# Kernel optimization log

Hardware: AMD Instinct MI355X
Metric: run time of the kernel (lower is better)

The kernel has to match this reference:

```python
import jax, jax.numpy as jnp
import numpy as np

B, L, E = 4, 2048, 1024
H, D = 16, 64  # heads, head_dim; H*D == E


def setup_inputs() -> dict:
    key = jax.random.key(0)
    ks = jax.random.split(key, 6)
    s = 0.02
    return {
        "x": jax.random.normal(ks[0], (B, L, E), dtype=jnp.float32),
        "Wq": jax.random.normal(ks[1], (E, H * D), dtype=jnp.float32) * s,
        "Wk": jax.random.normal(ks[2], (E, H * D), dtype=jnp.float32) * s,
        "Wv": jax.random.normal(ks[3], (E, H * D), dtype=jnp.float32) * s,
        "Wo": jax.random.normal(ks[4], (H * D, E), dtype=jnp.float32) * s,
        "bo": jax.random.normal(ks[5], (E,), dtype=jnp.float32) * s,
    }


def reference(x, Wq, Wk, Wv, Wo, bo):
    b, l, e = x.shape
    q = (x @ Wq).reshape(b, l, H, D)
    k = (x @ Wk).reshape(b, l, H, D)
    v = (x @ Wv).reshape(b, l, H, D)
    # NOTE: original scales by sqrt(embed_size), not sqrt(head_dim)
    energy = jnp.einsum('nqhd,nkhd->nhqk', q, k)
    attn = jax.nn.softmax(energy / jnp.sqrt(jnp.float32(e)), axis=3)
    out = jnp.einsum('nhql,nlhd->nqhd', attn, v).reshape(b, l, H * D)
    return out @ Wo + bo
```

## Files before the change

kernel.cpp:

```cpp
#include <hip/hip_runtime.h>

#define B_ 4
#define L_ 2048
#define E_ 1024
#define H_ 16
#define D_ 64
#define CSCALE 0.045084960222629414f

typedef short s16x8 __attribute__((ext_vector_type(8)));
typedef short s16x4 __attribute__((ext_vector_type(4)));
typedef float f32x4 __attribute__((ext_vector_type(4)));

__device__ __forceinline__ unsigned short f2bf(float f) {
  union { float f; unsigned int u; } v;
  v.f = f;
  unsigned int u = v.u;
  u += 0x7fffu + ((u >> 16) & 1u);
  return (unsigned short)(u >> 16);
}

__device__ __forceinline__ void async16(const void* g, void* l) {
  __builtin_amdgcn_global_load_lds(
      (__attribute__((address_space(1))) void*)(g),
      (__attribute__((address_space(3))) void*)(l), 16, 0, 0);
}

__global__ void k_prep(const float* __restrict__ x,
                       const float* __restrict__ Wq, const float* __restrict__ Wk,
                       const float* __restrict__ Wv, const float* __restrict__ Wo,
                       unsigned short* __restrict__ xb,
                       unsigned short* __restrict__ Wt, unsigned short* __restrict__ WoT) {
  __shared__ float t[32][33];
  int bid = blockIdx.x, tid = threadIdx.x;
  if (bid < 8192) {
    int i = bid * 256 + tid;
    float4 v = ((const float4*)x)[i];
    ushort4 o;
    o.x = f2bf(v.x); o.y = f2bf(v.y); o.z = f2bf(v.z); o.w = f2bf(v.w);
    ((ushort4*)xb)[i] = o;
    return;
  }
  int tt = bid - 8192;
  int wsel = tt >> 10, tile = tt & 1023;
  const float* in = (wsel == 0) ? Wq : (wsel == 1) ? Wk : (wsel == 2) ? Wv : Wo;
  unsigned short* out = (wsel == 0) ? Wt : (wsel == 1) ? Wt + (1u << 20)
                        : (wsel == 2) ? Wt + (2u << 20) : WoT;
  int bx = tile & 31, by = tile >> 5;
  int tx = tid & 31, ty = tid >> 5;
  int xcol = bx * 32 + tx;
  int y0 = by * 32;
#pragma unroll
  for (int i = 0; i < 4; ++i)
    t[ty + i * 8][tx] = in[(size_t)(y0 + ty + i * 8) * 1024 + xcol];
  __syncthreads();
  int xo = by * 32 + tx;
  int yo0 = bx * 32;
#pragma unroll
  for (int i = 0; i < 4; ++i)
    out[(size_t)(yo0 + ty + i * 8) * 1024 + xo] = f2bf(t[tx][ty + i * 8]);
}

__global__ __launch_bounds__(256) void k_gemm_qkvt(
    const unsigned short* __restrict__ xb, const unsigned short* __restrict__ Wt,
    unsigned short* __restrict__ Qb, unsigned short* __restrict__ Kb,
    unsigned short* __restrict__ Vt) {
  __shared__ __align__(16) unsigned short As[128 * 32];
  __shared__ __align__(16) unsigned short Bs[128 * 32];
  const int bid = blockIdx.x;
  const int tid = threadIdx.x;
  const int w = tid >> 6, lane = tid & 63;
  const int quad = lane >> 4, mrow = lane & 15;
  const bool isQK = bid < 1024;
  int m0, n0;
  const unsigned short *PA, *PB;
  if (isQK) {
    m0 = (bid & 63) * 128;
    n0 = (bid >> 6) * 128;
    PA = xb + (size_t)m0 * 1024;
    PB = Wt + (size_t)n0 * 1024;
  } else {
    int g = bid - 1024;
    m0 = (g & 7) * 128;
    n0 = (g >> 3) * 128;
    PA = Wt + (2u << 20) + (size_t)m0 * 1024;
    PB = xb + (size_t)n0 * 1024;
  }
  const int wr = (w >> 1) * 64, wc = (w & 1) * 64;
  const f32x4 fz = {0.f, 0.f, 0.f, 0.f};
  f32x4 acc[4][4];
#pragma unroll
  for (int a = 0; a < 4; ++a)
#pragma unroll
    for (int b = 0; b < 4; ++b) acc[a][b] = fz;

  for (int kt = 0; kt < 32; ++kt) {
    __syncthreads();
#pragma unroll
    for (int r = 0; r < 2; ++r) {
      int c = r * 256 + tid;
      int row = c >> 2, cc = c & 3;
      async16(PA + (size_t)row * 1024 + kt * 32 + cc * 8, &As[c * 8]);
    }
#pragma unroll
    for (int r = 0; r < 2; ++r) {
      int c = r * 256 + tid;
      int row = c >> 2, cc = c & 3;
      async16(PB + (size_t)row * 1024 + kt * 32 + cc * 8, &Bs[c * 8]);
    }
    __syncthreads();
    s16x8 a[4], b[4];
#pragma unroll
    for (int mt = 0; mt < 4; ++mt)
      a[mt] = *(const s16x8*)&As[(wr + mt * 16 + mrow) * 32 + quad * 8];
#pragma unroll
    for (int nt = 0; nt < 4; ++nt)
      b[nt] = *(const s16x8*)&Bs[(wc + nt * 16 + mrow) * 32 + quad * 8];
#pragma unroll
    for (int mt = 0; mt < 4; ++mt)
#pragma unroll
      for (int nt = 0; nt < 4; ++nt)
        acc[mt][nt] = __builtin_amdgcn_mfma_f32_16x16x32_bf16(a[mt], b[nt], acc[mt][nt], 0, 0, 0);
  }
  if (isQK) {
#pragma unroll
    for (int mt = 0; mt < 4; ++mt)
#pragma unroll
      for (int nt = 0; nt < 4; ++nt)
#pragma unroll
        for (int i = 0; i < 4; ++i) {
          int row = m0 + wr + mt * 16 + quad * 4 + i;
          int col = n0 + wc + nt * 16 + mrow;
          int bb = row >> 11, l = row & 2047;
          if (col < 1024) {
            int h = col >> 6, d = col & 63;
            Qb[(((size_t)(bb * 16 + h)) * 2048 + l) * 64 + d] = f2bf(acc[mt][nt][i]);
          } else {
            int c2 = col - 1024, h = c2 >> 6, d = c2 & 63;
            Kb[(((size_t)(bb * 16 + h)) * 2048 + l) * 64 + d] = f2bf(acc[mt][nt][i] * CSCALE);
          }
        }
  } else {
#pragma unroll
    for (int mt = 0; mt < 4; ++mt)
#pragma unroll
      for (int nt = 0; nt < 4; ++nt)
#pragma unroll
        for (int i = 0; i < 4; ++i) {
          int f = m0 + wr + mt * 16 + quad * 4 + i;
          int tk = n0 + wc + nt * 16 + mrow;
          int bb = tk >> 11, l = tk & 2047;
          Vt[((size_t)(bb * 1024 + f)) * 2048 + l] = f2bf(acc[mt][nt][i]);
        }
  }
}

__global__ __launch_bounds__(512, 4) void k_attn(
    const unsigned short* __restrict__ Qb, const unsigned short* __restrict__ Kb,
    const unsigned short* __restrict__ Vt, unsigned short* __restrict__ AO) {
  __shared__ __align__(16) unsigned short KVs[2][8192];
  const int tid = threadIdx.x, w = tid >> 6, lane = tid & 63;
  const int quad = lane >> 4, mrow = lane & 15;
  const int bh = blockIdx.y;
  const int q0 = blockIdx.x * 256;
  const unsigned short* Qh = Qb + (size_t)bh * 2048 * 64;
  const unsigned short* Kh = Kb + (size_t)bh * 2048 * 64;
  const unsigned short* Vh = Vt + (size_t)bh * 64 * 2048;
  unsigned short* KVf = &KVs[0][0];

#pragma unroll
  for (int r = 0; r < 4; ++r) {
    int c = r * 512 + tid;
    int row = c >> 3, cl = c & 7;
    int gc = cl ^ (row & 7);
    async16(Qh + (size_t)(q0 + row) * 64 + gc * 8, &KVf[c * 8]);
  }
  __syncthreads();
  s16x8 qb[2][2];
#pragma unroll
  for (int nt = 0; nt < 2; ++nt)
#pragma unroll
    for (int ks = 0; ks < 2; ++ks) {
      int row = w * 32 + nt * 16 + mrow;
      qb[nt][ks] = *(const s16x8*)&KVf[row * 64 + (((ks * 4 + quad) ^ (row & 7)) << 3)];
    }
  __syncthreads();

  {
    int c = tid;
    int row = c >> 3, cl = c & 7;
    int gc = cl ^ (row & 7);
    async16(Kh + (size_t)row * 64 + gc * 8, &KVs[0][c * 8]);
    async16(Vh + (size_t)row * 2048 + gc * 8, &KVs[0][4096 + c * 8]);
  }

  const f32x4 fz = {0.f, 0.f, 0.f, 0.f};
  f32x4 o[2][4];
  float lr[2];
#pragma unroll
  for (int nt = 0; nt < 2; ++nt) {
    lr[nt] = 0.f;
#pragma unroll
    for (int dt = 0; dt < 4; ++dt) o[nt][dt] = fz;
  }

  for (int j = 0; j < 32; ++j) {
    __syncthreads();
    const unsigned short* Kt = &KVs[j & 1][0];
    const unsigned short* Vs = &KVs[j & 1][4096];

    s16x8 ak[4][2];
#pragma unroll
    for (int mt = 0; mt < 4; ++mt)
#pragma unroll
      for (int ks = 0; ks < 2; ++ks) {
        int row = mt * 16 + mrow;
        ak[mt][ks] = *(const s16x8*)&Kt[row * 64 + (((ks * 4 + quad) ^ (row & 7)) << 3)];
      }
    s16x4 vb[4][4];
#pragma unroll
    for (int dt = 0; dt < 4; ++dt)
#pragma unroll
      for (int lt = 0; lt < 4; ++lt) {
        int row = dt * 16 + mrow;
        int lbase = lt * 16 + quad * 4;
        int cg = lbase >> 3, off = lbase & 7;
        vb[dt][lt] = *(const s16x4*)&Vs[row * 64 + ((cg ^ (row & 7)) << 3) + off];
      }

    if (j + 1 < 32) {
      unsigned short* nb = &KVs[(j + 1) & 1][0];
      int c = tid;
      int row = c >> 3, cl = c & 7;
      int gc = cl ^ (row & 7);
      async16(Kh + (size_t)((j + 1) * 64 + row) * 64 + gc * 8, &nb[c * 8]);
      async16(Vh + (size_t)row * 2048 + (j + 1) * 64 + gc * 8, &nb[4096 + c * 8]);
    }

    f32x4 s[4][2];
#pragma unroll
    for (int mt = 0; mt < 4; ++mt)
#pragma unroll
      for (int nt = 0; nt < 2; ++nt) s[mt][nt] = fz;
    __builtin_amdgcn_s_setprio(1);
#pragma unroll
    for (int ks = 0; ks < 2; ++ks)
#pragma unroll
      for (int mt = 0; mt < 4; ++mt)
#pragma unroll
        for (int nt = 0; nt < 2; ++nt)
          s[mt][nt] = __builtin_amdgcn_mfma_f32_16x16x32_bf16(ak[mt][ks], qb[nt][ks], s[mt][nt], 0, 0, 0);
    __builtin_amdgcn_s_setprio(0);

    s16x4 pa[4][2];
#pragma unroll
    for (int mt = 0; mt < 4; ++mt)
#pragma unroll
      for (int nt = 0; nt < 2; ++nt) {
        float p0 = __builtin_amdgcn_exp2f(s[mt][nt][0]);
        float p1 = __builtin_amdgcn_exp2f(s[mt][nt][1]);
        float p2 = __builtin_amdgcn_exp2f(s[mt][nt][2]);
        float p3 = __builtin_amdgcn_exp2f(s[mt][nt][3]);
        lr[nt] += (p0 + p1) + (p2 + p3);
        unsigned int r01, r23;
        asm("v_cvt_pk_bf16_f32 %0, %1, %2" : "=v"(r01) : "v"(p0), "v"(p1));
        asm("v_cvt_pk_bf16_f32 %0, %1, %2" : "=v"(r23) : "v"(p2), "v"(p3));
        union { unsigned int u[2]; s16x4 v4; } uu;
        uu.u[0] = r01; uu.u[1] = r23;
        pa[mt][nt] = uu.v4;
      }

    __builtin_amdgcn_s_setprio(1);
#pragma unroll
    for (int nt = 0; nt < 2; ++nt)
#pragma unroll
      for (int dt = 0; dt < 4; ++dt)
#pragma unroll
        for (int lt = 0; lt < 4; ++lt)
          o[nt][dt] = __builtin_amdgcn_mfma_f32_16x16x16bf16_1k(pa[lt][nt], vb[dt][lt], o[nt][dt], 0, 0, 0);
    __builtin_amdgcn_s_setprio(0);
  }

#pragma unroll
  for (int nt = 0; nt < 2; ++nt) {
    float v = lr[nt];
    v += __shfl_xor(v, 16);
    v += __shfl_xor(v, 32);
    lr[nt] = v;
  }

  int b_ = bh >> 4, h = bh & 15;
#pragma unroll
  for (int nt = 0; nt < 2; ++nt)
#pragma unroll
    for (int i = 0; i < 4; ++i) {
      float inv = 1.f / __shfl(lr[nt], quad * 4 + i, 64);
      int qrow = q0 + w * 32 + nt * 16 + quad * 4 + i;
#pragma unroll
      for (int dt = 0; dt < 4; ++dt) {
        int d = dt * 16 + mrow;
        AO[((size_t)(b_ * 2048 + qrow)) * 1024 + h * 64 + d] = f2bf(o[nt][dt][i] * inv);
      }
    }
}

__global__ __launch_bounds__(256) void k_gemm_out(
    const unsigned short* __restrict__ Ab, const unsigned short* __restrict__ WoT,
    const float* __restrict__ bo, float* __restrict__ out) {
  __shared__ __align__(16) unsigned short As[128 * 32];
  __shared__ __align__(16) unsigned short Bs[128 * 32];
  const int tid = threadIdx.x;
  const int w = tid >> 6, lane = tid & 63;
  const int quad = lane >> 4, mrow = lane & 15;
  const int m0 = blockIdx.x * 128, n0 = blockIdx.y * 128;
  const int wr = (w >> 1) * 64, wc = (w & 1) * 64;
  const f32x4 fz = {0.f, 0.f, 0.f, 0.f};
  f32x4 acc[4][4];
#pragma unroll
  for (int a = 0; a < 4; ++a)
#pragma unroll
    for (int b = 0; b < 4; ++b) acc[a][b] = fz;

  for (int kt = 0; kt < 32; ++kt) {
    __syncthreads();
#pragma unroll
    for (int r = 0; r < 2; ++r) {
      int c = r * 256 + tid;
      int row = c >> 2, cc = c & 3;
      async16(Ab + (size_t)(m0 + row) * 1024 + kt * 32 + cc * 8, &As[c * 8]);
    }
#pragma unroll
    for (int r = 0; r < 2; ++r) {
      int c = r * 256 + tid;
      int row = c >> 2, cc = c & 3;
      async16(WoT + (size_t)(n0 + row) * 1024 + kt * 32 + cc * 8, &Bs[c * 8]);
    }
    __syncthreads();
    s16x8 a[4], b[4];
#pragma unroll
    for (int mt = 0; mt < 4; ++mt)
      a[mt] = *(const s16x8*)&As[(wr + mt * 16 + mrow) * 32 + quad * 8];
#pragma unroll
    for (int nt = 0; nt < 4; ++nt)
      b[nt] = *(const s16x8*)&Bs[(wc + nt * 16 + mrow) * 32 + quad * 8];
#pragma unroll
    for (int mt = 0; mt < 4; ++mt)
#pragma unroll
      for (int nt = 0; nt < 4; ++nt)
        acc[mt][nt] = __builtin_amdgcn_mfma_f32_16x16x32_bf16(a[mt], b[nt], acc[mt][nt], 0, 0, 0);
  }
#pragma unroll
  for (int mt = 0; mt < 4; ++mt)
#pragma unroll
    for (int nt = 0; nt < 4; ++nt)
#pragma unroll
      for (int i = 0; i < 4; ++i) {
        int row = m0 + wr + mt * 16 + quad * 4 + i;
        int col = n0 + wc + nt * 16 + mrow;
        out[(size_t)row * 1024 + col] = acc[mt][nt][i] + bo[col];
      }
}

extern "C" void kernel_launch(void* const* d_in, const int* in_sizes, int n_in,
                              void* d_out, int out_size, void* d_ws, size_t ws_size,
                              hipStream_t stream) {
  const float* x  = (const float*)d_in[0];
  const float* Wq = (const float*)d_in[1];
  const float* Wk = (const float*)d_in[2];
  const float* Wv = (const float*)d_in[3];
  const float* Wo = (const float*)d_in[4];
  const float* bo = (const float*)d_in[5];
  float* out = (float*)d_out;

  char* ws = (char*)d_ws;
  const size_t MiB = 1u << 20;
  unsigned short* xb  = (unsigned short*)(ws);
  unsigned short* Wt  = (unsigned short*)(ws + 16 * MiB);
  unsigned short* WoT = (unsigned short*)(ws + 22 * MiB);
  unsigned short* Qb  = (unsigned short*)(ws + 24 * MiB);
  unsigned short* Kb  = (unsigned short*)(ws + 40 * MiB);
  unsigned short* Vt  = (unsigned short*)(ws + 56 * MiB);
  unsigned short* AO  = xb;

  k_prep<<<12288, 256, 0, stream>>>(x, Wq, Wk, Wv, Wo, xb, Wt, WoT);
  k_gemm_qkvt<<<1536, 256, 0, stream>>>(xb, Wt, Qb, Kb, Vt);
  k_attn<<<dim3(8, 64), 512, 0, stream>>>(Qb, Kb, Vt, AO);
  k_gemm_out<<<dim3(64, 8), 256, 0, stream>>>(AO, WoT, bo, out);
}
```

Before: 319.3 us.

## Halve attention block to 256 threads and interleave LDS loads with MFMAs

The attention kernel now uses 256-thread blocks that each cover 128 query rows, doubling the grid to 16x64 blocks. Each thread issues two async copies per KV tile to fill the same 64-key buffer. The inner loop loads K fragments per key subtile and V fragments per key chunk right before their MFMAs, instead of preloading whole tiles into registers. This is meant to cut register pressure and let more blocks run at once, at the cost of more K/V tile traffic per query and less load-ahead.

```diff
diff --git a/kernel.cpp b/kernel.cpp
--- a/kernel.cpp
+++ b/kernel.cpp
@@ -154,14 +154,14 @@
   }
 }
 
-__global__ __launch_bounds__(512, 4) void k_attn(
+__global__ __launch_bounds__(256, 4) void k_attn(
     const unsigned short* __restrict__ Qb, const unsigned short* __restrict__ Kb,
     const unsigned short* __restrict__ Vt, unsigned short* __restrict__ AO) {
   __shared__ __align__(16) unsigned short KVs[2][8192];
   const int tid = threadIdx.x, w = tid >> 6, lane = tid & 63;
   const int quad = lane >> 4, mrow = lane & 15;
   const int bh = blockIdx.y;
-  const int q0 = blockIdx.x * 256;
+  const int q0 = blockIdx.x * 128;
   const unsigned short* Qh = Qb + (size_t)bh * 2048 * 64;
   const unsigned short* Kh = Kb + (size_t)bh * 2048 * 64;
   const unsigned short* Vh = Vt + (size_t)bh * 64 * 2048;
@@ -169,7 +169,7 @@
 
 #pragma unroll
   for (int r = 0; r < 4; ++r) {
-    int c = r * 512 + tid;
+    int c = r * 256 + tid;
     int row = c >> 3, cl = c & 7;
     int gc = cl ^ (row & 7);
     async16(Qh + (size_t)(q0 + row) * 64 + gc * 8, &KVf[c * 8]);
@@ -185,8 +185,9 @@
     }
   __syncthreads();
 
-  {
-    int c = tid;
+#pragma unroll
+  for (int r = 0; r < 2; ++r) {
+    int c = r * 256 + tid;
     int row = c >> 3, cl = c & 7;
     int gc = cl ^ (row & 7);
     async16(Kh + (size_t)row * 64 + gc * 8, &KVs[0][c * 8]);
@@ -208,58 +209,38 @@
     const unsigned short* Kt = &KVs[j & 1][0];
     const unsigned short* Vs = &KVs[j & 1][4096];
 
-    s16x8 ak[4][2];
-#pragma unroll
-    for (int mt = 0; mt < 4; ++mt)
-#pragma unroll
-      for (int ks = 0; ks < 2; ++ks) {
-        int row = mt * 16 + mrow;
-        ak[mt][ks] = *(const s16x8*)&Kt[row * 64 + (((ks * 4 + quad) ^ (row & 7)) << 3)];
-      }
-    s16x4 vb[4][4];
-#pragma unroll
-    for (int dt = 0; dt < 4; ++dt)
-#pragma unroll
-      for (int lt = 0; lt < 4; ++lt) {
-        int row = dt * 16 + mrow;
-        int lbase = lt * 16 + quad * 4;
-        int cg = lbase >> 3, off = lbase & 7;
-        vb[dt][lt] = *(const s16x4*)&Vs[row * 64 + ((cg ^ (row & 7)) << 3) + off];
-      }
-
     if (j + 1 < 32) {
       unsigned short* nb = &KVs[(j + 1) & 1][0];
-      int c = tid;
-      int row = c >> 3, cl = c & 7;
-      int gc = cl ^ (row & 7);
-      async16(Kh + (size_t)((j + 1) * 64 + row) * 64 + gc * 8, &nb[c * 8]);
-      async16(Vh + (size_t)row * 2048 + (j + 1) * 64 + gc * 8, &nb[4096 + c * 8]);
-    }
-
-    f32x4 s[4][2];
-#pragma unroll
-    for (int mt = 0; mt < 4; ++mt)
-#pragma unroll
-      for (int nt = 0; nt < 2; ++nt) s[mt][nt] = fz;
-    __builtin_amdgcn_s_setprio(1);
-#pragma unroll
-    for (int ks = 0; ks < 2; ++ks)
-#pragma unroll
-      for (int mt = 0; mt < 4; ++mt)
-#pragma unroll
-        for (int nt = 0; nt < 2; ++nt)
-          s[mt][nt] = __builtin_amdgcn_mfma_f32_16x16x32_bf16(ak[mt][ks], qb[nt][ks], s[mt][nt], 0, 0, 0);
-    __builtin_amdgcn_s_setprio(0);
+#pragma unroll
+      for (int r = 0; r < 2; ++r) {
+        int c = r * 256 + tid;
+        int row = c >> 3, cl = c & 7;
+        int gc = cl ^ (row & 7);
+        async16(Kh + (size_t)((j + 1) * 64 + row) * 64 + gc * 8, &nb[c * 8]);
+        async16(Vh + (size_t)row * 2048 + (j + 1) * 64 + gc * 8, &nb[4096 + c * 8]);
+      }
+    }
 
     s16x4 pa[4][2];
 #pragma unroll
-    for (int mt = 0; mt < 4; ++mt)
+    for (int mt = 0; mt < 4; ++mt) {
+      int row = mt * 16 + mrow;
+      s16x8 ak0 = *(const s16x8*)&Kt[row * 64 + (((0 * 4 + quad) ^ (row & 7)) << 3)];
+      s16x8 ak1 = *(const s16x8*)&Kt[row * 64 + (((1 * 4 + quad) ^ (row & 7)) << 3)];
+      f32x4 s0 = fz, s1 = fz;
+      __builtin_amdgcn_s_setprio(1);
+      s0 = __builtin_amdgcn_mfma_f32_16x16x32_bf16(ak0, qb[0][0], s0, 0, 0, 0);
+      s1 = __builtin_amdgcn_mfma_f32_16x16x32_bf16(ak0, qb[1][0], s1, 0, 0, 0);
+      s0 = __builtin_amdgcn_mfma_f32_16x16x32_bf16(ak1, qb[0][1], s0, 0, 0, 0);
+      s1 = __builtin_amdgcn_mfma_f32_16x16x32_bf16(ak1, qb[1][1], s1, 0, 0, 0);
+      __builtin_amdgcn_s_setprio(0);
 #pragma unroll
       for (int nt = 0; nt < 2; ++nt) {
-        float p0 = __builtin_amdgcn_exp2f(s[mt][nt][0]);
-        float p1 = __builtin_amdgcn_exp2f(s[mt][nt][1]);
-        float p2 = __builtin_amdgcn_exp2f(s[mt][nt][2]);
-        float p3 = __builtin_amdgcn_exp2f(s[mt][nt][3]);
+        const f32x4 sv = nt ? s1 : s0;
+        float p0 = __builtin_amdgcn_exp2f(sv[0]);
+        float p1 = __builtin_amdgcn_exp2f(sv[1]);
+        float p2 = __builtin_amdgcn_exp2f(sv[2]);
+        float p3 = __builtin_amdgcn_exp2f(sv[3]);
         lr[nt] += (p0 + p1) + (p2 + p3);
         unsigned int r01, r23;
         asm("v_cvt_pk_bf16_f32 %0, %1, %2" : "=v"(r01) : "v"(p0), "v"(p1));
@@ -268,16 +249,26 @@
         uu.u[0] = r01; uu.u[1] = r23;
         pa[mt][nt] = uu.v4;
       }
-
-    __builtin_amdgcn_s_setprio(1);
-#pragma unroll
-    for (int nt = 0; nt < 2; ++nt)
-#pragma unroll
-      for (int dt = 0; dt < 4; ++dt)
-#pragma unroll
-        for (int lt = 0; lt < 4; ++lt)
-          o[nt][dt] = __builtin_amdgcn_mfma_f32_16x16x16bf16_1k(pa[lt][nt], vb[dt][lt], o[nt][dt], 0, 0, 0);
-    __builtin_amdgcn_s_setprio(0);
+    }
+
+#pragma unroll
+    for (int lt = 0; lt < 4; ++lt) {
+      s16x4 vb[4];
+      int lbase = lt * 16 + quad * 4;
+      int cg = lbase >> 3, off = lbase & 7;
+#pragma unroll
+      for (int dt = 0; dt < 4; ++dt) {
+        int row = dt * 16 + mrow;
+        vb[dt] = *(const s16x4*)&Vs[row * 64 + ((cg ^ (row & 7)) << 3) + off];
+      }
+      __builtin_amdgcn_s_setprio(1);
+#pragma unroll
+      for (int nt = 0; nt < 2; ++nt)
+#pragma unroll
+        for (int dt = 0; dt < 4; ++dt)
+          o[nt][dt] = __builtin_amdgcn_mfma_f32_16x16x16bf16_1k(pa[lt][nt], vb[dt], o[nt][dt], 0, 0, 0);
+      __builtin_amdgcn_s_setprio(0);
+    }
   }
 
 #pragma unroll
@@ -383,6 +374,6 @@
 
   k_prep<<<12288, 256, 0, stream>>>(x, Wq, Wk, Wv, Wo, xb, Wt, WoT);
   k_gemm_qkvt<<<1536, 256, 0, stream>>>(xb, Wt, Qb, Kb, Vt);
-  k_attn<<<dim3(8, 64), 512, 0, stream>>>(Qb, Kb, Vt, AO);
+  k_attn<<<dim3(16, 64), 256, 0, stream>>>(Qb, Kb, Vt, AO);
   k_gemm_out<<<dim3(64, 8), 256, 0, stream>>>(AO, WoT, bo, out);
 }
```

Result: faster. 276.4 us (-13.5%).
